# Kernel optimization log

Measured on AMD Instinct MI355X. Metric: run time of the kernel, lower is better.

Reference implementation:

```python
import jax, jax.numpy as jnp
import numpy as np

N = 100000
E = 2000000
IN_DIM = 5
D = 32
L = 3
EPS = 1e-5


def setup_inputs() -> dict:
    key = jax.random.key(0)
    ks = jax.random.split(key, 10)
    x = jax.random.normal(ks[0], (N, IN_DIM), dtype=jnp.float32)
    edge_index = jax.random.randint(ks[1], (2, E), 0, N, dtype=jnp.int64)
    s = 1.0 / np.sqrt(D)
    w_in = jax.random.normal(ks[2], (D, IN_DIM), dtype=jnp.float32) / np.sqrt(IN_DIM)
    b_in = jnp.zeros((D,), dtype=jnp.float32)
    w_l = jax.random.normal(ks[3], (L, D, D), dtype=jnp.float32) * s  # lin_l per layer
    b_l = jnp.zeros((L, D), dtype=jnp.float32)
    w_r = jax.random.normal(ks[4], (L, D, D), dtype=jnp.float32) * s  # lin_r per layer (no bias, as in PyG SAGEConv)
    gamma = jnp.ones((D,), dtype=jnp.float32)
    beta = jnp.zeros((D,), dtype=jnp.float32)
    return {"x": x, "edge_index": edge_index, "w_in": w_in, "b_in": b_in,
            "w_l": w_l, "b_l": b_l, "w_r": w_r, "gamma": gamma, "beta": beta}


def _layernorm(h, gamma, beta):
    mu = jnp.mean(h, axis=-1, keepdims=True)
    var = jnp.mean(jnp.square(h - mu), axis=-1, keepdims=True)
    return (h - mu) * jax.lax.rsqrt(var + EPS) * gamma + beta


def reference(x, edge_index, w_in, b_in, w_l, b_l, w_r, gamma, beta):
    src = edge_index[0]
    dst = edge_index[1]
    n = x.shape[0]
    # node in-degree for mean aggregation (0-degree nodes get 0 output, like scatter_mean)
    deg = jax.ops.segment_sum(jnp.ones((src.shape[0],), dtype=x.dtype), dst, num_segments=n)
    inv_deg = (1.0 / jnp.maximum(deg, 1.0))[:, None]  # [N,1]
    h = x @ w_in.T + b_in  # [N, D]
    for i in range(w_l.shape[0]):
        msg = h[src]  # [E, D] gather
        agg = jax.ops.segment_sum(msg, dst, num_segments=n) * inv_deg  # mean aggregate
        h = agg @ w_l[i].T + b_l[i] + h @ w_r[i].T  # SAGEConv: lin_l(aggr) + lin_r(x)
        h = _layernorm(jax.nn.relu(h), gamma, beta)
    return h
```

## Files before the change

kernel.cpp:

```cpp
#include <hip/hip_runtime.h>
#include <hip/hip_bf16.h>

#define DIM 32
#define INDIM 5
#define EPB 4096
#define BKBITS 7
#define BKN 128
#define NBMAX 1024
#define CAP 4096

__device__ __forceinline__ unsigned short f2bf(float f) {
    unsigned u = __float_as_uint(f);
    u += 0x7FFFu + ((u >> 16) & 1u);
    return (unsigned short)(u >> 16);
}
__device__ __forceinline__ float bf2f_lo(unsigned u) { return __uint_as_float(u << 16); }
__device__ __forceinline__ float bf2f_hi(unsigned u) { return __uint_as_float(u & 0xFFFF0000u); }


__global__ __launch_bounds__(256) void bucket_count_kernel(const int* __restrict__ dst,
                                                           int* __restrict__ bcnt, int e, int nb) {
    __shared__ int hist[NBMAX];
    int t = threadIdx.x;
    for (int i = t; i < nb; i += 256) hist[i] = 0;
    __syncthreads();
    int base = blockIdx.x * EPB;
    for (int k = 0; k < EPB; k += 256) {
        int i = base + k + t;
        if (i < e) {
            int dv = __builtin_nontemporal_load(&dst[i]);
            atomicAdd(&hist[dv >> BKBITS], 1);
        }
    }
    __syncthreads();
    for (int i = t; i < nb; i += 256) {
        int h = hist[i];
        if (h) atomicAdd(&bcnt[i], h);
    }
}


__global__ void bucket_scan_kernel(const int* __restrict__ bcnt, int* __restrict__ bbase,
                                   int* __restrict__ bcur, int* __restrict__ row_ptr,
                                   int nb, int n, int e) {
    __shared__ int s[1024];
    int t = threadIdx.x;
    int v = (t < nb) ? bcnt[t] : 0;
    s[t] = v;
    __syncthreads();
    for (int o = 1; o < 1024; o <<= 1) {
        int a = (t >= o) ? s[t - o] : 0;
        __syncthreads();
        s[t] += a;
        __syncthreads();
    }
    if (t < nb) {
        int excl = s[t] - v;
        bbase[t] = excl;
        bcur[t] = excl;
    }
    if (t == 0) {
        bbase[nb] = e;
        row_ptr[n] = e;
    }
}


__global__ __launch_bounds__(256) void bucket_fill_kernel(const int* __restrict__ src,
                                                          const int* __restrict__ dst,
                                                          int* __restrict__ bcur,
                                                          unsigned* __restrict__ packed,
                                                          int e, int nb) {
    __shared__ unsigned sw[EPB];
    __shared__ unsigned short sb[EPB];
    __shared__ int hist[NBMAX];
    __shared__ int rbase[NBMAX];
    int t = threadIdx.x;
    for (int i = t; i < nb; i += 256) hist[i] = 0;
    __syncthreads();
    int base = blockIdx.x * EPB;
    for (int k = 0; k < EPB; k += 256) {
        int i = base + k + t;
        if (i < e) {
            int s = __builtin_nontemporal_load(&src[i]);
            int d = __builtin_nontemporal_load(&dst[i]);
            int b = d >> BKBITS;
            sw[k + t] = ((unsigned)s << BKBITS) | (unsigned)(d & (BKN - 1));
            sb[k + t] = (unsigned short)b;
            atomicAdd(&hist[b], 1);
        }
    }
    __syncthreads();
    for (int i = t; i < nb; i += 256) {
        int h = hist[i];
        rbase[i] = h ? atomicAdd(&bcur[i], h) : 0;
        hist[i] = 0;
    }
    __syncthreads();
    for (int k = 0; k < EPB; k += 256) {
        int i = base + k + t;
        if (i < e) {
            int b = sb[k + t];
            int r = atomicAdd(&hist[b], 1);
            packed[rbase[b] + r] = sw[k + t];
        }
    }
}


__global__ __launch_bounds__(256) void csr_build_kernel(const unsigned* __restrict__ packed,
                                                        const int* __restrict__ bbase,
                                                        int* __restrict__ row_ptr,
                                                        int* __restrict__ esrc, int n) {
    __shared__ unsigned ew[CAP];
    __shared__ int h2[BKN];
    __shared__ int off[BKN];
    int b = blockIdx.x;
    int base = bbase[b];
    int cnt = bbase[b + 1] - base;
    int t = threadIdx.x;
    if (t < BKN) h2[t] = 0;
    __syncthreads();
    bool staged = (cnt <= CAP);
    for (int i = t; i < cnt; i += 256) {
        unsigned w = __builtin_nontemporal_load(&packed[base + i]);
        if (staged) ew[i] = w;
        atomicAdd(&h2[w & (BKN - 1)], 1);
    }
    __syncthreads();
    int v = 0;
    if (t < BKN) {
        v = h2[t];
        off[t] = v;
    }
    __syncthreads();
    for (int o = 1; o < BKN; o <<= 1) {
        int a = 0;
        if (t < BKN && t >= o) a = off[t - o];
        __syncthreads();
        if (t < BKN) off[t] += a;
        __syncthreads();
    }
    if (t < BKN) {
        int excl = off[t] - v;
        off[t] = excl;
        h2[t] = 0;
    }
    __syncthreads();
    int node = b * BKN + t;
    if (t < BKN && node < n) row_ptr[node] = base + off[t];
    for (int i = t; i < cnt; i += 256) {
        unsigned w = staged ? ew[i] : packed[base + i];
        int dl = w & (BKN - 1);
        int r = atomicAdd(&h2[dl], 1);
        esrc[base + off[dl] + r] = (int)(w >> BKBITS);
    }
}


__global__ void input_proj_kernel(const float* __restrict__ x, const float* __restrict__ w_in,
                                  const float* __restrict__ b_in,
                                  unsigned short* __restrict__ h, int n) {
    __shared__ float sw[DIM * INDIM];
    __shared__ float sb[DIM];
    int t = threadIdx.x;
    if (t < DIM * INDIM) sw[t] = w_in[t];
    if (t < DIM) sb[t] = b_in[t];
    __syncthreads();
    int idx = blockIdx.x * 256 + t;
    int node = idx >> 5;
    int d = idx & 31;
    if (node < n) {
        const float* xr = x + (size_t)node * INDIM;
        float acc = sb[d];
#pragma unroll
        for (int k = 0; k < INDIM; k++) acc = fmaf(xr[k], sw[d * INDIM + k], acc);
        h[(size_t)(d >> 4) * n * 16 + (size_t)node * 16 + (d & 15)] = f2bf(acc);
    }
}


template <int LAST>
__global__ __launch_bounds__(128, 4) void layer_fused_kernel(
    const int* __restrict__ row_ptr, const int* __restrict__ esrc,
    const unsigned short* __restrict__ h_in,
    unsigned short* __restrict__ h_out_bf, float* __restrict__ out_f32,
    const float* __restrict__ wl, const float* __restrict__ bl,
    const float* __restrict__ wr, const float* __restrict__ gamma,
    const float* __restrict__ beta, int n) {
    __shared__ float sAgg[32][DIM];
    __shared__ float sSelf[32][DIM];

    int t = threadIdx.x;
    int d = t & 31;
    int nd = t >> 2;
    int q = t & 3;
    int node = blockIdx.x * 32 + nd;

    int rs = 0, re = 0;
    if (node < n) {
        rs = row_ptr[node];
        re = row_ptr[node + 1];
    }
    float iv = 1.f / fmaxf((float)(re - rs), 1.f);

#pragma unroll
    for (int p = 0; p < 2; ++p) {
        const uint2* hv = (const uint2*)(h_in + (size_t)p * n * 16);
        if (node < n) {
            {
                uint2 v = hv[(size_t)node * 4 + q];
                float4 f = make_float4(bf2f_lo(v.x), bf2f_hi(v.x), bf2f_lo(v.y), bf2f_hi(v.y));
                *(float4*)&sSelf[nd][p * 16 + q * 4] = f;
            }
            float a0 = 0.f, a1 = 0.f, a2 = 0.f, a3 = 0.f;
            int j = rs;
            int i0, i1, i2, i3, i4, i5, i6, i7;
            bool have = (j + 8 <= re);
            if (have) {
                i0 = esrc[j];     i1 = esrc[j + 1]; i2 = esrc[j + 2]; i3 = esrc[j + 3];
                i4 = esrc[j + 4]; i5 = esrc[j + 5]; i6 = esrc[j + 6]; i7 = esrc[j + 7];
            }
            while (have) {
                int jn = j + 8;
                bool haven = (jn + 8 <= re);
                int t0, t1, t2, t3, t4, t5, t6, t7;
                if (haven) {
                    t0 = esrc[jn];     t1 = esrc[jn + 1]; t2 = esrc[jn + 2]; t3 = esrc[jn + 3];
                    t4 = esrc[jn + 4]; t5 = esrc[jn + 5]; t6 = esrc[jn + 6]; t7 = esrc[jn + 7];
                }
                uint2 v0 = hv[(size_t)i0 * 4 + q];
                uint2 v1 = hv[(size_t)i1 * 4 + q];
                uint2 v2 = hv[(size_t)i2 * 4 + q];
                uint2 v3 = hv[(size_t)i3 * 4 + q];
                uint2 v4 = hv[(size_t)i4 * 4 + q];
                uint2 v5 = hv[(size_t)i5 * 4 + q];
                uint2 v6 = hv[(size_t)i6 * 4 + q];
                uint2 v7 = hv[(size_t)i7 * 4 + q];
                a0 += bf2f_lo(v0.x); a1 += bf2f_hi(v0.x); a2 += bf2f_lo(v0.y); a3 += bf2f_hi(v0.y);
                a0 += bf2f_lo(v1.x); a1 += bf2f_hi(v1.x); a2 += bf2f_lo(v1.y); a3 += bf2f_hi(v1.y);
                a0 += bf2f_lo(v2.x); a1 += bf2f_hi(v2.x); a2 += bf2f_lo(v2.y); a3 += bf2f_hi(v2.y);
                a0 += bf2f_lo(v3.x); a1 += bf2f_hi(v3.x); a2 += bf2f_lo(v3.y); a3 += bf2f_hi(v3.y);
                a0 += bf2f_lo(v4.x); a1 += bf2f_hi(v4.x); a2 += bf2f_lo(v4.y); a3 += bf2f_hi(v4.y);
                a0 += bf2f_lo(v5.x); a1 += bf2f_hi(v5.x); a2 += bf2f_lo(v5.y); a3 += bf2f_hi(v5.y);
                a0 += bf2f_lo(v6.x); a1 += bf2f_hi(v6.x); a2 += bf2f_lo(v6.y); a3 += bf2f_hi(v6.y);
                a0 += bf2f_lo(v7.x); a1 += bf2f_hi(v7.x); a2 += bf2f_lo(v7.y); a3 += bf2f_hi(v7.y);
                j = jn;
                have = haven;
                if (haven) {
                    i0 = t0; i1 = t1; i2 = t2; i3 = t3; i4 = t4; i5 = t5; i6 = t6; i7 = t7;
                }
            }
            for (; j < re; ++j) {
                int s = esrc[j];
                uint2 v = hv[(size_t)s * 4 + q];
                a0 += bf2f_lo(v.x); a1 += bf2f_hi(v.x); a2 += bf2f_lo(v.y); a3 += bf2f_hi(v.y);
            }
            float4 f = make_float4(a0 * iv, a1 * iv, a2 * iv, a3 * iv);
            *(float4*)&sAgg[nd][p * 16 + q * 4] = f;
        }
    }
    __syncthreads();

    float wlr[DIM], wrr[DIM];
    {
        const float4* p1 = (const float4*)(wl + (size_t)d * DIM);
        const float4* p2 = (const float4*)(wr + (size_t)d * DIM);
#pragma unroll
        for (int qq = 0; qq < 8; qq++) {
            float4 a = p1[qq];
            wlr[4 * qq] = a.x; wlr[4 * qq + 1] = a.y; wlr[4 * qq + 2] = a.z; wlr[4 * qq + 3] = a.w;
            float4 c = p2[qq];
            wrr[4 * qq] = c.x; wrr[4 * qq + 1] = c.y; wrr[4 * qq + 2] = c.z; wrr[4 * qq + 3] = c.w;
        }
    }
    float bias = bl[d], g = gamma[d], be = beta[d];

#pragma unroll
    for (int it = 0; it < 8; ++it) {
        int ln = it * 4 + (t >> 5);
        int nodec = blockIdx.x * 32 + ln;
        if (nodec < n) {
            float o = bias;
            const float* va = sAgg[ln];
            const float* vs = sSelf[ln];
#pragma unroll
            for (int qq = 0; qq < 8; qq++) {
                float4 a = *(const float4*)&va[qq * 4];
                float4 s = *(const float4*)&vs[qq * 4];
                o = fmaf(a.x, wlr[4 * qq], o);     o = fmaf(s.x, wrr[4 * qq], o);
                o = fmaf(a.y, wlr[4 * qq + 1], o); o = fmaf(s.y, wrr[4 * qq + 1], o);
                o = fmaf(a.z, wlr[4 * qq + 2], o); o = fmaf(s.z, wrr[4 * qq + 2], o);
                o = fmaf(a.w, wlr[4 * qq + 3], o); o = fmaf(s.w, wrr[4 * qq + 3], o);
            }
            float out = fmaxf(o, 0.f);
            float sum = out, sq = out * out;
#pragma unroll
            for (int off = 16; off > 0; off >>= 1) {
                sum += __shfl_xor(sum, off, 32);
                sq += __shfl_xor(sq, off, 32);
            }
            float mu = sum * (1.f / 32.f);
            float var = fmaxf(sq * (1.f / 32.f) - mu * mu, 0.f);
            float r = rsqrtf(var + 1e-5f);
            float res = (out - mu) * r * g + be;
            if (LAST) out_f32[(size_t)nodec * DIM + d] = res;
            else      h_out_bf[(size_t)(d >> 4) * n * 16 + (size_t)nodec * 16 + (d & 15)] = f2bf(res);
        }
    }
}


extern "C" void kernel_launch(void* const* d_in, const int* in_sizes, int n_in,
                              void* d_out, int out_size, void* d_ws, size_t ws_size,
                              hipStream_t stream) {
    const float* x = (const float*)d_in[0];
    const int* ei = (const int*)d_in[1];
    const float* w_in = (const float*)d_in[2];
    const float* b_in = (const float*)d_in[3];
    const float* w_l = (const float*)d_in[4];
    const float* b_l = (const float*)d_in[5];
    const float* w_r = (const float*)d_in[6];
    const float* gamma = (const float*)d_in[7];
    const float* beta = (const float*)d_in[8];

    int n = in_sizes[0] / INDIM;
    int e = in_sizes[1] / 2;
    int L = in_sizes[4] / (DIM * DIM);
    const int* src = ei;
    const int* dst = ei + e;
    int nb = (n + BKN - 1) >> BKBITS;

    char* w = (char*)d_ws;
    int* bcnt = (int*)w;               w += (size_t)NBMAX * 4;
    int* bbase = (int*)w;              w += (size_t)(NBMAX + 1) * 4;
    int* bcur = (int*)w;               w += (size_t)NBMAX * 4;
    int* row_ptr = (int*)w;            w += (size_t)(n + 1) * 4;
    int* esrc = (int*)w;               w += (size_t)e * 4;
    unsigned short* h_A = (unsigned short*)w;  w += (size_t)n * DIM * 2;
    unsigned short* h_B = (unsigned short*)w;  w += (size_t)n * DIM * 2;
    unsigned* packed = (unsigned*)h_A;

    int nbE = (e + EPB - 1) / EPB;

    hipMemsetAsync(bcnt, 0, (size_t)nb * 4, stream);
    bucket_count_kernel<<<nbE, 256, 0, stream>>>(dst, bcnt, e, nb);
    bucket_scan_kernel<<<1, 1024, 0, stream>>>(bcnt, bbase, bcur, row_ptr, nb, n, e);
    bucket_fill_kernel<<<nbE, 256, 0, stream>>>(src, dst, bcur, packed, e, nb);
    csr_build_kernel<<<nb, 256, 0, stream>>>(packed, bbase, row_ptr, esrc, n);

    input_proj_kernel<<<(n * DIM + 255) / 256, 256, 0, stream>>>(x, w_in, b_in, h_A, n);

    unsigned short* bufs[2] = {h_A, h_B};
    int nbF = (n + 31) / 32;
    for (int i = 0; i < L; i++) {
        const unsigned short* hin = bufs[i & 1];
        unsigned short* hout = bufs[(i + 1) & 1];
        const float* wl = w_l + (size_t)i * DIM * DIM;
        const float* bl = b_l + (size_t)i * DIM;
        const float* wr = w_r + (size_t)i * DIM * DIM;
        if (i == L - 1)
            layer_fused_kernel<1><<<nbF, 128, 0, stream>>>(row_ptr, esrc, hin, nullptr,
                                                           (float*)d_out, wl, bl, wr,
                                                           gamma, beta, n);
        else
            layer_fused_kernel<0><<<nbF, 128, 0, stream>>>(row_ptr, esrc, hin, hout,
                                                           nullptr, wl, bl, wr,
                                                           gamma, beta, n);
    }
}
```

Baseline: 273.7 us.

## Use row-major bf16 features with single-pass 16-byte gathers and packed adds

Switches the bf16 hidden-state layout from two 16-wide planes to one contiguous 64-byte row per node. Each node's neighbours are now gathered in a single pass with uint4 loads instead of two passes over the edge list, halving esrc reads and the number of gather instructions. The edge loop is unrolled to 16 loads in flight with an 8-edge tail, and accumulation uses inline v_pk_add_f32. Occupancy hint drops from 4 to 3 blocks per CU to make room for the extra registers, which risks less latency hiding.

```diff
diff --git a/kernel.cpp b/kernel.cpp
--- a/kernel.cpp
+++ b/kernel.cpp
@@ -16,6 +16,19 @@
 }
 __device__ __forceinline__ float bf2f_lo(unsigned u) { return __uint_as_float(u << 16); }
 __device__ __forceinline__ float bf2f_hi(unsigned u) { return __uint_as_float(u & 0xFFFF0000u); }
+
+__device__ __forceinline__ void acc_pk(float2& a01, float2& a23, float2& a45, float2& a67,
+                                       uint4 v) {
+    float2 v01, v23, v45, v67;
+    v01.x = bf2f_lo(v.x); v01.y = bf2f_hi(v.x);
+    v23.x = bf2f_lo(v.y); v23.y = bf2f_hi(v.y);
+    v45.x = bf2f_lo(v.z); v45.y = bf2f_hi(v.z);
+    v67.x = bf2f_lo(v.w); v67.y = bf2f_hi(v.w);
+    asm volatile("v_pk_add_f32 %0, %0, %1" : "+v"(a01) : "v"(v01));
+    asm volatile("v_pk_add_f32 %0, %0, %1" : "+v"(a23) : "v"(v23));
+    asm volatile("v_pk_add_f32 %0, %0, %1" : "+v"(a45) : "v"(v45));
+    asm volatile("v_pk_add_f32 %0, %0, %1" : "+v"(a67) : "v"(v67));
+}
 
 
 __global__ __launch_bounds__(256) void bucket_count_kernel(const int* __restrict__ dst,
@@ -175,13 +188,13 @@
         float acc = sb[d];
 #pragma unroll
         for (int k = 0; k < INDIM; k++) acc = fmaf(xr[k], sw[d * INDIM + k], acc);
-        h[(size_t)(d >> 4) * n * 16 + (size_t)node * 16 + (d & 15)] = f2bf(acc);
+        h[(size_t)node * DIM + d] = f2bf(acc);
     }
 }
 
 
 template <int LAST>
-__global__ __launch_bounds__(128, 4) void layer_fused_kernel(
+__global__ __launch_bounds__(128, 3) void layer_fused_kernel(
     const int* __restrict__ row_ptr, const int* __restrict__ esrc,
     const unsigned short* __restrict__ h_in,
     unsigned short* __restrict__ h_out_bf, float* __restrict__ out_f32,
@@ -193,72 +206,72 @@
 
     int t = threadIdx.x;
     int d = t & 31;
+
     int nd = t >> 2;
     int q = t & 3;
     int node = blockIdx.x * 32 + nd;
-
-    int rs = 0, re = 0;
+    const uint4* hv = (const uint4*)h_in;
+
     if (node < n) {
-        rs = row_ptr[node];
-        re = row_ptr[node + 1];
-    }
-    float iv = 1.f / fmaxf((float)(re - rs), 1.f);
-
-#pragma unroll
-    for (int p = 0; p < 2; ++p) {
-        const uint2* hv = (const uint2*)(h_in + (size_t)p * n * 16);
-        if (node < n) {
-            {
-                uint2 v = hv[(size_t)node * 4 + q];
-                float4 f = make_float4(bf2f_lo(v.x), bf2f_hi(v.x), bf2f_lo(v.y), bf2f_hi(v.y));
-                *(float4*)&sSelf[nd][p * 16 + q * 4] = f;
+        {
+            uint4 v = hv[(size_t)node * 4 + q];
+            float4 f0 = make_float4(bf2f_lo(v.x), bf2f_hi(v.x), bf2f_lo(v.y), bf2f_hi(v.y));
+            float4 f1 = make_float4(bf2f_lo(v.z), bf2f_hi(v.z), bf2f_lo(v.w), bf2f_hi(v.w));
+            *(float4*)&sSelf[nd][q * 8] = f0;
+            *(float4*)&sSelf[nd][q * 8 + 4] = f1;
+        }
+        int rs = row_ptr[node];
+        int re = row_ptr[node + 1];
+        float2 a01 = make_float2(0.f, 0.f), a23 = make_float2(0.f, 0.f);
+        float2 a45 = make_float2(0.f, 0.f), a67 = make_float2(0.f, 0.f);
+        int j = rs;
+        int ids[16];
+        bool have = (j + 16 <= re);
+        if (have) {
+#pragma unroll
+            for (int k = 0; k < 16; k++) ids[k] = esrc[j + k];
+        }
+        while (have) {
+            int jn = j + 16;
+            bool haven = (jn + 16 <= re);
+            uint4 vv[16];
+#pragma unroll
+            for (int k = 0; k < 16; k++) vv[k] = hv[(size_t)ids[k] * 4 + q];
+            int nids[16];
+            if (haven) {
+#pragma unroll
+                for (int k = 0; k < 16; k++) nids[k] = esrc[jn + k];
             }
-            float a0 = 0.f, a1 = 0.f, a2 = 0.f, a3 = 0.f;
-            int j = rs;
-            int i0, i1, i2, i3, i4, i5, i6, i7;
-            bool have = (j + 8 <= re);
-            if (have) {
-                i0 = esrc[j];     i1 = esrc[j + 1]; i2 = esrc[j + 2]; i3 = esrc[j + 3];
-                i4 = esrc[j + 4]; i5 = esrc[j + 5]; i6 = esrc[j + 6]; i7 = esrc[j + 7];
+#pragma unroll
+            for (int k = 0; k < 16; k++) acc_pk(a01, a23, a45, a67, vv[k]);
+            j = jn;
+            have = haven;
+            if (haven) {
+#pragma unroll
+                for (int k = 0; k < 16; k++) ids[k] = nids[k];
             }
-            while (have) {
-                int jn = j + 8;
-                bool haven = (jn + 8 <= re);
-                int t0, t1, t2, t3, t4, t5, t6, t7;
-                if (haven) {
-                    t0 = esrc[jn];     t1 = esrc[jn + 1]; t2 = esrc[jn + 2]; t3 = esrc[jn + 3];
-                    t4 = esrc[jn + 4]; t5 = esrc[jn + 5]; t6 = esrc[jn + 6]; t7 = esrc[jn + 7];
-                }
-                uint2 v0 = hv[(size_t)i0 * 4 + q];
-                uint2 v1 = hv[(size_t)i1 * 4 + q];
-                uint2 v2 = hv[(size_t)i2 * 4 + q];
-                uint2 v3 = hv[(size_t)i3 * 4 + q];
-                uint2 v4 = hv[(size_t)i4 * 4 + q];
-                uint2 v5 = hv[(size_t)i5 * 4 + q];
-                uint2 v6 = hv[(size_t)i6 * 4 + q];
-                uint2 v7 = hv[(size_t)i7 * 4 + q];
-                a0 += bf2f_lo(v0.x); a1 += bf2f_hi(v0.x); a2 += bf2f_lo(v0.y); a3 += bf2f_hi(v0.y);
-                a0 += bf2f_lo(v1.x); a1 += bf2f_hi(v1.x); a2 += bf2f_lo(v1.y); a3 += bf2f_hi(v1.y);
-                a0 += bf2f_lo(v2.x); a1 += bf2f_hi(v2.x); a2 += bf2f_lo(v2.y); a3 += bf2f_hi(v2.y);
-                a0 += bf2f_lo(v3.x); a1 += bf2f_hi(v3.x); a2 += bf2f_lo(v3.y); a3 += bf2f_hi(v3.y);
-                a0 += bf2f_lo(v4.x); a1 += bf2f_hi(v4.x); a2 += bf2f_lo(v4.y); a3 += bf2f_hi(v4.y);
-                a0 += bf2f_lo(v5.x); a1 += bf2f_hi(v5.x); a2 += bf2f_lo(v5.y); a3 += bf2f_hi(v5.y);
-                a0 += bf2f_lo(v6.x); a1 += bf2f_hi(v6.x); a2 += bf2f_lo(v6.y); a3 += bf2f_hi(v6.y);
-                a0 += bf2f_lo(v7.x); a1 += bf2f_hi(v7.x); a2 += bf2f_lo(v7.y); a3 += bf2f_hi(v7.y);
-                j = jn;
-                have = haven;
-                if (haven) {
-                    i0 = t0; i1 = t1; i2 = t2; i3 = t3; i4 = t4; i5 = t5; i6 = t6; i7 = t7;
-                }
-            }
-            for (; j < re; ++j) {
-                int s = esrc[j];
-                uint2 v = hv[(size_t)s * 4 + q];
-                a0 += bf2f_lo(v.x); a1 += bf2f_hi(v.x); a2 += bf2f_lo(v.y); a3 += bf2f_hi(v.y);
-            }
-            float4 f = make_float4(a0 * iv, a1 * iv, a2 * iv, a3 * iv);
-            *(float4*)&sAgg[nd][p * 16 + q * 4] = f;
-        }
+        }
+        if (j + 8 <= re) {
+            int id8[8];
+#pragma unroll
+            for (int k = 0; k < 8; k++) id8[k] = esrc[j + k];
+            uint4 vv[8];
+#pragma unroll
+            for (int k = 0; k < 8; k++) vv[k] = hv[(size_t)id8[k] * 4 + q];
+#pragma unroll
+            for (int k = 0; k < 8; k++) acc_pk(a01, a23, a45, a67, vv[k]);
+            j += 8;
+        }
+        for (; j < re; ++j) {
+            int s = esrc[j];
+            uint4 v = hv[(size_t)s * 4 + q];
+            acc_pk(a01, a23, a45, a67, v);
+        }
+        float iv = 1.f / fmaxf((float)(re - rs), 1.f);
+        float4 f0 = make_float4(a01.x * iv, a01.y * iv, a23.x * iv, a23.y * iv);
+        float4 f1 = make_float4(a45.x * iv, a45.y * iv, a67.x * iv, a67.y * iv);
+        *(float4*)&sAgg[nd][q * 8] = f0;
+        *(float4*)&sAgg[nd][q * 8 + 4] = f1;
     }
     __syncthreads();
 
@@ -305,7 +318,7 @@
             float r = rsqrtf(var + 1e-5f);
             float res = (out - mu) * r * g + be;
             if (LAST) out_f32[(size_t)nodec * DIM + d] = res;
-            else      h_out_bf[(size_t)(d >> 4) * n * 16 + (size_t)nodec * 16 + (d & 15)] = f2bf(res);
+            else      h_out_bf[(size_t)nodec * DIM + d] = f2bf(res);
         }
     }
 }
```

Result: faster. 246.1 us (-10.1%).
